# Kernel optimization log

Hardware: AMD Instinct MI355X
Metric: run time of the kernel (lower is better)

Reference implementation:

```python
import jax, jax.numpy as jnp
import numpy as np

W_RNN = 768
DEC_H = 256
TAGS = 2
TAG_EM = 32


def setup_inputs() -> dict:
    key = jax.random.key(0)
    ks = jax.random.split(key, 8)
    B, T = 64, 512
    in_size = W_RNN + TAG_EM  # 800
    aff_in = W_RNN + DEC_H    # 1024
    sents_vec = jax.random.normal(ks[0], (B, T, W_RNN), dtype=jnp.float32)
    mask_cls = jnp.ones((B, T), dtype=jnp.float32)
    # xavier-uniform-ish init for weights, zeros for biases (matches param_init)
    def xavier(k, shape):
        fan_in, fan_out = shape[1], shape[0]
        lim = float(np.sqrt(6.0 / (fan_in + fan_out)))
        return jax.random.uniform(k, shape, jnp.float32, -lim, lim)
    Wih = xavier(ks[1], (4 * DEC_H, in_size))
    Whh = xavier(ks[2], (4 * DEC_H, DEC_H))
    bih = jnp.zeros((4 * DEC_H,), jnp.float32)
    bhh = jnp.zeros((4 * DEC_H,), jnp.float32)
    Waff = xavier(ks[3], (TAGS, aff_in))
    baff = jnp.zeros((TAGS,), jnp.float32)
    tag_em = xavier(ks[4], (TAGS, TAG_EM))
    return {"sents_vec": sents_vec, "mask_cls": mask_cls, "Wih": Wih,
            "Whh": Whh, "bih": bih, "bhh": bhh, "Waff": Waff,
            "baff": baff, "tag_em": tag_em}


def reference(sents_vec, mask_cls, Wih, Whh, bih, bhh, Waff, baff, tag_em):
    # Dropout is treated in eval mode (identity), as is standard for a
    # deterministic correctness baseline.
    B, T, D = sents_vec.shape
    H = DEC_H
    h0 = jnp.zeros((B, H), sents_vec.dtype)
    go = jnp.zeros((B, TAG_EM), sents_vec.dtype)

    Hs = jnp.swapaxes(sents_vec, 0, 1)        # [T, B, D]
    Ms = jnp.swapaxes(mask_cls, 0, 1)[..., None]  # [T, B, 1]

    def step(carry, xs):
        h, c, yem = carry
        Hi, mi = xs
        x = jnp.concatenate([yem, Hi], axis=1)            # [B, 800]
        gates = x @ Wih.T + h @ Whh.T + (bih + bhh)       # [B, 4H]
        i_g, f_g, g_g, o_g = jnp.split(gates, 4, axis=1)  # torch LSTMCell order
        c_new = jax.nn.sigmoid(f_g) * c + jax.nn.sigmoid(i_g) * jnp.tanh(g_g)
        h_new = jax.nn.sigmoid(o_g) * jnp.tanh(c_new)
        score = jnp.concatenate([h_new, Hi], axis=1) @ Waff.T + baff  # [B, TAGS]
        pred = jnp.argmax(score, axis=-1)                 # [B]
        yem_new = tag_em[pred]                            # [B, TAG_EM]
        h_out = h_new * mi + h * (1.0 - mi)
        c_out = c_new * mi + c * (1.0 - mi)
        return (h_out, c_out, yem_new), score

    _, scores = jax.lax.scan(step, (h0, h0, go), (Hs, Ms))  # [T, B, TAGS]
    scores = jnp.swapaxes(scores, 0, 1)                      # [B, T, TAGS]
    return jax.nn.log_softmax(scores, axis=2)
```

## Files before the change

kernel.cpp:

```cpp
#include <hip/hip_runtime.h>
#include <cstdint>
#include <cstddef>

#define TT 512
#define BB 64
#define HH 256
#define NG 1024
#define DI 768
#define KY 32

#define LDP 56

typedef __attribute__((ext_vector_type(8))) short bfrag_t;
typedef __attribute__((ext_vector_type(4))) float f4_t;

__device__ __forceinline__ float sigf(float x) {
    return __fdividef(1.f, 1.f + __expf(-x));
}
__device__ __forceinline__ float tanhfast(float x) {
    return fmaf(2.f, sigf(2.f * x), -1.f);
}
__device__ __forceinline__ unsigned short bf_hi(float x) {
    return (unsigned short)(__float_as_uint(x) >> 16);
}
__device__ __forceinline__ float bf_hi_f(float x) {
    return __uint_as_float(__float_as_uint(x) & 0xffff0000u);
}

__global__ __launch_bounds__(256) void kgemm2(
    const float* __restrict__ sents, const float* __restrict__ Wih,
    const float* __restrict__ bih, const float* __restrict__ bhh,
    float* __restrict__ gpre, int t0)
{
    __shared__ unsigned short Ah[128 * LDP], Al[128 * LDP];
    __shared__ unsigned short Bh[128 * LDP], Bl[128 * LDP];

    const int tid = threadIdx.x;
    const int nb = blockIdx.x;
    const int mb = blockIdx.y;
    const int wv = tid >> 6, lane = tid & 63;
    const int wm = (wv >> 1) * 64, wn = (wv & 1) * 64;
    const int fl = lane & 15, quad = lane >> 4;

    f4_t acc[4][4];
#pragma unroll
    for (int mi = 0; mi < 4; ++mi)
#pragma unroll
        for (int ni = 0; ni < 4; ++ni) acc[mi][ni] = (f4_t)0.f;

    const int sr = tid >> 1, sk = (tid & 1) * 16;
    const int gr = mb * 128 + sr;
    const float* aptr = sents + ((size_t)(gr & 63) * TT + t0 + (gr >> 6)) * DI + sk;
    const float* bptr = Wih + (size_t)(nb * 128 + sr) * 800 + KY + sk;

    for (int k0 = 0; k0 < DI; k0 += 32) {
        float4 av[4], bv[4];
#pragma unroll
        for (int i = 0; i < 4; ++i) {
            av[i] = *(const float4*)(aptr + k0 + i * 4);
            bv[i] = *(const float4*)(bptr + k0 + i * 4);
        }
        __syncthreads();
#pragma unroll
        for (int i = 0; i < 4; ++i) {
            ushort4 h4, l4;
            h4.x = bf_hi(av[i].x); l4.x = bf_hi(av[i].x - bf_hi_f(av[i].x));
            h4.y = bf_hi(av[i].y); l4.y = bf_hi(av[i].y - bf_hi_f(av[i].y));
            h4.z = bf_hi(av[i].z); l4.z = bf_hi(av[i].z - bf_hi_f(av[i].z));
            h4.w = bf_hi(av[i].w); l4.w = bf_hi(av[i].w - bf_hi_f(av[i].w));
            *(ushort4*)&Ah[sr * LDP + sk + i * 4] = h4;
            *(ushort4*)&Al[sr * LDP + sk + i * 4] = l4;
            h4.x = bf_hi(bv[i].x); l4.x = bf_hi(bv[i].x - bf_hi_f(bv[i].x));
            h4.y = bf_hi(bv[i].y); l4.y = bf_hi(bv[i].y - bf_hi_f(bv[i].y));
            h4.z = bf_hi(bv[i].z); l4.z = bf_hi(bv[i].z - bf_hi_f(bv[i].z));
            h4.w = bf_hi(bv[i].w); l4.w = bf_hi(bv[i].w - bf_hi_f(bv[i].w));
            *(ushort4*)&Bh[sr * LDP + sk + i * 4] = h4;
            *(ushort4*)&Bl[sr * LDP + sk + i * 4] = l4;
        }
        __syncthreads();

        bfrag_t ah[4], al2[4], bh[4], bl2[4];
#pragma unroll
        for (int mi = 0; mi < 4; ++mi) {
            int row = wm + mi * 16 + fl;
            ah[mi]  = *(const bfrag_t*)&Ah[row * LDP + quad * 8];
            al2[mi] = *(const bfrag_t*)&Al[row * LDP + quad * 8];
        }
#pragma unroll
        for (int ni = 0; ni < 4; ++ni) {
            int col = wn + ni * 16 + fl;
            bh[ni]  = *(const bfrag_t*)&Bh[col * LDP + quad * 8];
            bl2[ni] = *(const bfrag_t*)&Bl[col * LDP + quad * 8];
        }
#pragma unroll
        for (int mi = 0; mi < 4; ++mi)
#pragma unroll
            for (int ni = 0; ni < 4; ++ni) {
                acc[mi][ni] = __builtin_amdgcn_mfma_f32_16x16x32_bf16(
                    ah[mi], bh[ni], acc[mi][ni], 0, 0, 0);
                acc[mi][ni] = __builtin_amdgcn_mfma_f32_16x16x32_bf16(
                    ah[mi], bl2[ni], acc[mi][ni], 0, 0, 0);
                acc[mi][ni] = __builtin_amdgcn_mfma_f32_16x16x32_bf16(
                    al2[mi], bh[ni], acc[mi][ni], 0, 0, 0);
            }
    }

#pragma unroll
    for (int ni = 0; ni < 4; ++ni) {
        int gcol = nb * 128 + wn + ni * 16 + fl;
        float bias = bih[gcol] + bhh[gcol];
#pragma unroll
        for (int mi = 0; mi < 4; ++mi) {
            int grow = mb * 128 + wm + mi * 16 + quad * 4;
#pragma unroll
            for (int r = 0; r < 4; ++r)
                gpre[(size_t)(grow + r) * NG + gcol] = acc[mi][ni][r] + bias;
        }
    }
}

__global__ __launch_bounds__(256) void kshi(
    const float* __restrict__ sents, const float* __restrict__ Waff,
    const float* __restrict__ baff, float* __restrict__ shi, int t0)
{
    const int tid = threadIdx.x;
    const int lane = tid & 63;
    const int r = blockIdx.x * 4 + (tid >> 6);
    const int b = r & 63, tl = r >> 6;
    const float* hi = sents + ((size_t)b * TT + t0 + tl) * DI;
    float p0 = 0.f, p1 = 0.f;
#pragma unroll
    for (int kk = 0; kk < 12; ++kk) {
        int k = kk * 64 + lane;
        float x = hi[k];
        p0 = fmaf(x, Waff[HH + k], p0);
        p1 = fmaf(x, Waff[NG + HH + k], p1);
    }
#pragma unroll
    for (int off = 32; off >= 1; off >>= 1) {
        p0 += __shfl_xor(p0, off, 64);
        p1 += __shfl_xor(p1, off, 64);
    }
    if (lane == 0) {
        shi[(size_t)r * 2 + 0] = p0 + baff[0];
        shi[(size_t)r * 2 + 1] = p1 + baff[1];
    }
}

__global__ void kinit(unsigned long long* __restrict__ hbox) {
    hbox[(size_t)blockIdx.x * 512 + threadIdx.x] = 0ull;
}

__global__ __launch_bounds__(512, 1) void krec3(
    const float* __restrict__ gpre,
    const float* __restrict__ shi,
    const float* __restrict__ Whh,
    const float* __restrict__ mask,
    float* __restrict__ out,
    float* __restrict__ sh, float* __restrict__ sc, int* __restrict__ sp,
    unsigned long long* __restrict__ hbox,
    const float* __restrict__ Wih, const float* __restrict__ tag,
    const float* __restrict__ Waff,
    int t0, int Tc, int first)
{
    const int blk = blockIdx.x;
    const int g = blk >> 6, b = blk & 63;
    const int tid = threadIdx.x;
    const int w = tid >> 6, lane = tid & 63;
    const int jl = lane & 7, kq = lane >> 3;
    const int jh = w * 8 + jl;
    const int jglob = g * 64 + jh;

    __shared__ float hk[8 * 36];
    __shared__ float hnS[HH];
    __shared__ float P[2][4][64];
    __shared__ float tg[2][KY];
    __shared__ float red[8][2];

    float4 wreg[4][8];
#pragma unroll
    for (int gt = 0; gt < 4; ++gt) {
        const float4* src = (const float4*)(Whh + (size_t)(gt * HH + jglob) * HH + kq * 32);
#pragma unroll
        for (int kk = 0; kk < 8; ++kk) wreg[gt][kk] = src[kk];
    }

    const int sdim = w * 32 + (lane & 31);
    const int stag = lane >> 5;
    const float waffR = Waff[(size_t)stag * NG + sdim];

    if (tid < 2 * KY) tg[tid >> 5][tid & 31] = tag[tid];
    __syncthreads();
    {
        int r = tid >> 8, rem = tid & 255, gt = rem >> 6, j2 = rem & 63;
        int row = gt * HH + g * 64 + j2;
        const float4* wr = (const float4*)(Wih + (size_t)row * 800);
        float s = 0.f;
#pragma unroll
        for (int kk = 0; kk < 8; ++kk) {
            float4 v = wr[kk];
            s = fmaf(v.x, tg[r][kk * 4 + 0], s);
            s = fmaf(v.y, tg[r][kk * 4 + 1], s);
            s = fmaf(v.z, tg[r][kk * 4 + 2], s);
            s = fmaf(v.w, tg[r][kk * 4 + 3], s);
        }
        P[r][gt][j2] = s;
    }

    float creg; int pred;
    if (first) {
        creg = 0.f; pred = -1;
        if (tid < 72) ((float4*)hk)[tid] = make_float4(0.f, 0.f, 0.f, 0.f);
    } else {
        creg = sc[(size_t)b * HH + jglob];
        pred = sp[b];
        if (tid < HH) hk[(tid >> 5) * 36 + (tid & 31)] = sh[(size_t)b * HH + tid];
    }
    __syncthreads();

    float cgp0, cgp1, cgp2, cgp3, cmi, cs0, cs1;
    {
        const float* gp = gpre + ((size_t)0 * BB + b) * NG;
        cgp0 = gp[0 * HH + jglob]; cgp1 = gp[1 * HH + jglob];
        cgp2 = gp[2 * HH + jglob]; cgp3 = gp[3 * HH + jglob];
        cmi = mask[(size_t)b * TT + t0];
        const float* s2 = shi + ((size_t)0 * BB + b) * 2;
        cs0 = s2[0]; cs1 = s2[1];
    }

    for (int tl = 0; tl < Tc; ++tl) {
        const int t = t0 + tl;
        const int p = t & 1;

        float pv0 = 0.f, pv1 = 0.f, pv2 = 0.f, pv3 = 0.f;
        if (pred >= 0) {
            pv0 = P[pred][0][jh]; pv1 = P[pred][1][jh];
            pv2 = P[pred][2][jh]; pv3 = P[pred][3][jh];
        }

        float a0 = 0.f, a1 = 0.f, a2 = 0.f, a3 = 0.f;
        const float4* h4 = (const float4*)(hk + kq * 36);
#pragma unroll
        for (int kk = 0; kk < 8; ++kk) {
            float4 hv = h4[kk];
            a0 = fmaf(wreg[0][kk].x, hv.x, a0); a0 = fmaf(wreg[0][kk].y, hv.y, a0);
            a0 = fmaf(wreg[0][kk].z, hv.z, a0); a0 = fmaf(wreg[0][kk].w, hv.w, a0);
            a1 = fmaf(wreg[1][kk].x, hv.x, a1); a1 = fmaf(wreg[1][kk].y, hv.y, a1);
            a1 = fmaf(wreg[1][kk].z, hv.z, a1); a1 = fmaf(wreg[1][kk].w, hv.w, a1);
            a2 = fmaf(wreg[2][kk].x, hv.x, a2); a2 = fmaf(wreg[2][kk].y, hv.y, a2);
            a2 = fmaf(wreg[2][kk].z, hv.z, a2); a2 = fmaf(wreg[2][kk].w, hv.w, a2);
            a3 = fmaf(wreg[3][kk].x, hv.x, a3); a3 = fmaf(wreg[3][kk].y, hv.y, a3);
            a3 = fmaf(wreg[3][kk].z, hv.z, a3); a3 = fmaf(wreg[3][kk].w, hv.w, a3);
        }
        a0 += __shfl_xor(a0, 8, 64); a0 += __shfl_xor(a0, 16, 64); a0 += __shfl_xor(a0, 32, 64);
        a1 += __shfl_xor(a1, 8, 64); a1 += __shfl_xor(a1, 16, 64); a1 += __shfl_xor(a1, 32, 64);
        a2 += __shfl_xor(a2, 8, 64); a2 += __shfl_xor(a2, 16, 64); a2 += __shfl_xor(a2, 32, 64);
        a3 += __shfl_xor(a3, 8, 64); a3 += __shfl_xor(a3, 16, 64); a3 += __shfl_xor(a3, 32, 64);

        float gi = a0 + cgp0 + pv0;
        float gf = a1 + cgp1 + pv1;
        float gg = a2 + cgp2 + pv2;
        float go = a3 + cgp3 + pv3;
        float ig = sigf(gi), fg = sigf(gf);
        float g2 = tanhfast(gg), og = sigf(go);
        float cn = fmaf(fg, creg, ig * g2);
        float hn = og * tanhfast(cn);
        float mi = cmi;
        float s2v0 = cs0, s2v1 = cs1;
        creg = cn * mi + creg * (1.f - mi);

        if (kq == 0) {
            unsigned long long wd =
                ((unsigned long long)__float_as_uint(hn) << 32) | (unsigned)(t + 1);
            __hip_atomic_store(&hbox[((size_t)(p * BB + b) * 4 + g) * 64 + jh], wd,
                               __ATOMIC_RELAXED, __HIP_MEMORY_SCOPE_AGENT);
            hnS[jglob] = hn;
        }

        if (tl + 1 < Tc) {
            const float* gp2 = gpre + ((size_t)(tl + 1) * BB + b) * NG;
            cgp0 = gp2[0 * HH + jglob]; cgp1 = gp2[1 * HH + jglob];
            cgp2 = gp2[2 * HH + jglob]; cgp3 = gp2[3 * HH + jglob];
            cmi = mask[(size_t)b * TT + t + 1];
            const float* s2n = shi + ((size_t)(tl + 1) * BB + b) * 2;
            cs0 = s2n[0]; cs1 = s2n[1];
        }

        if (tid < 192) {
            int pg = (g + 1 + (tid >> 6)) & 3, j2 = tid & 63;
            const unsigned long long* wp = &hbox[((size_t)(p * BB + b) * 4 + pg) * 64 + j2];
            unsigned long long wv;
            do {
                wv = __hip_atomic_load(wp, __ATOMIC_RELAXED, __HIP_MEMORY_SCOPE_AGENT);
            } while ((unsigned)wv != (unsigned)(t + 1));
            hnS[pg * 64 + j2] = __uint_as_float((unsigned)(wv >> 32));
        }
        __syncthreads();

        if (tid < HH) {
            int idx = (tid >> 5) * 36 + (tid & 31);
            float hold = hk[idx];
            hk[idx] = hnS[tid] * mi + hold * (1.f - mi);
        }
        float prod = hnS[sdim] * waffR;
        prod += __shfl_xor(prod, 1, 64);
        prod += __shfl_xor(prod, 2, 64);
        prod += __shfl_xor(prod, 4, 64);
        prod += __shfl_xor(prod, 8, 64);
        prod += __shfl_xor(prod, 16, 64);
        if ((lane & 31) == 0) red[w][stag] = prod;
        __syncthreads();

        float s0 = red[0][0];
        s0 += red[1][0]; s0 += red[2][0]; s0 += red[3][0];
        s0 += red[4][0]; s0 += red[5][0]; s0 += red[6][0]; s0 += red[7][0];
        float s1 = red[0][1];
        s1 += red[1][1]; s1 += red[2][1]; s1 += red[3][1];
        s1 += red[4][1]; s1 += red[5][1]; s1 += red[6][1]; s1 += red[7][1];
        float ts0 = s0 + s2v0, ts1 = s1 + s2v1;
        pred = (ts1 > ts0) ? 1 : 0;
        if (g == 0 && tid == 0) {
            float m = fmaxf(ts0, ts1);
            float lse = m + log1pf(expf(-fabsf(ts0 - ts1)));
            float* op = out + ((size_t)b * TT + t) * 2;
            op[0] = ts0 - lse; op[1] = ts1 - lse;
        }
    }

    if (kq == 0) {
        sh[(size_t)b * HH + jglob] = hk[(jglob >> 5) * 36 + (jglob & 31)];
        sc[(size_t)b * HH + jglob] = creg;
    }
    if (g == 0 && tid == 0) sp[b] = pred;
}

extern "C" void kernel_launch(void* const* d_in, const int* in_sizes, int n_in,
                              void* d_out, int out_size, void* d_ws, size_t ws_size,
                              hipStream_t stream) {
    (void)in_sizes; (void)n_in; (void)out_size;
    const float* sents = (const float*)d_in[0];
    const float* mask  = (const float*)d_in[1];
    const float* Wih   = (const float*)d_in[2];
    const float* Whh   = (const float*)d_in[3];
    const float* bih   = (const float*)d_in[4];
    const float* bhh   = (const float*)d_in[5];
    const float* Waff  = (const float*)d_in[6];
    const float* baff  = (const float*)d_in[7];
    const float* tag   = (const float*)d_in[8];
    float* out = (float*)d_out;

    const size_t fixed = (size_t)BB * HH * 4 * 2
                       + BB * 4
                       + (size_t)2 * BB * 4 * 64 * 8
                       + 4096;
    int Tc = 8;
    const int cands[7] = {512, 256, 128, 64, 32, 16, 8};
    for (int i = 0; i < 7; ++i) {
        size_t need = (size_t)cands[i] * BB * NG * 4
                    + (size_t)cands[i] * BB * 2 * 4
                    + fixed;
        if (need <= ws_size) { Tc = cands[i]; break; }
    }

    char* wsp = (char*)d_ws;
    float* gpre = (float*)wsp; wsp += (size_t)Tc * BB * NG * 4;
    float* shiw = (float*)wsp; wsp += (size_t)Tc * BB * 2 * 4;
    float* shst = (float*)wsp; wsp += (size_t)BB * HH * 4;
    float* scst = (float*)wsp; wsp += (size_t)BB * HH * 4;
    int*   spst = (int*)wsp;   wsp += BB * 4;
    unsigned long long* hbox = (unsigned long long*)wsp;

    kinit<<<dim3(64), 512, 0, stream>>>(hbox);

    const int nch = TT / Tc;
    for (int c = 0; c < nch; ++c) {
        const int t0 = c * Tc;
        kgemm2<<<dim3(8, Tc * 64 / 128), 256, 0, stream>>>(sents, Wih, bih, bhh, gpre, t0);
        kshi<<<dim3(Tc * 16), 256, 0, stream>>>(sents, Waff, baff, shiw, t0);
        krec3<<<dim3(256), 512, 0, stream>>>(gpre, shiw, Whh, mask, out,
                                             shst, scst, spst, hbox,
                                             Wih, tag, Waff, t0, Tc, (c == 0) ? 1 : 0);
    }
}
```

Measured before the change: 1.436 ms.

## Exchange partial affine scores via mailboxes and double-buffer h to drop a barrier

The recurrent kernel now computes each block's partial affine score over its own 64 hidden units and publishes it through a new tagged mailbox. A dedicated wave collects the four partials, so the full tag decision no longer needs a second block-wide reduction and barrier. The hidden-state buffer in shared memory is double-buffered, and masked h values are kept in registers, which removes the separate mask-mix pass and one __syncthreads per timestep. The cost is extra global atomic stores and spin-loads per step, plus a slightly different summation order for the scores.

After: 1.617 ms. 1.13x slower.

```diff
diff --git a/kernel.cpp b/kernel.cpp
--- a/kernel.cpp
+++ b/kernel.cpp
@@ -19,6 +19,9 @@
 }
 __device__ __forceinline__ float tanhfast(float x) {
     return fmaf(2.f, sigf(2.f * x), -1.f);
+}
+__device__ __forceinline__ float hmix(float hn, float hold, float mi) {
+    return fmaf(hn, mi, hold * (1.f - mi));
 }
 __device__ __forceinline__ unsigned short bf_hi(float x) {
     return (unsigned short)(__float_as_uint(x) >> 16);
@@ -147,11 +150,11 @@
     }
 }
 
-__global__ void kinit(unsigned long long* __restrict__ hbox) {
-    hbox[(size_t)blockIdx.x * 512 + threadIdx.x] = 0ull;
-}
-
-__global__ __launch_bounds__(512, 1) void krec3(
+__global__ void kinit(unsigned long long* __restrict__ box) {
+    box[(size_t)blockIdx.x * 512 + threadIdx.x] = 0ull;
+}
+
+__global__ __launch_bounds__(512, 1) void krec4(
     const float* __restrict__ gpre,
     const float* __restrict__ shi,
     const float* __restrict__ Whh,
@@ -159,6 +162,7 @@
     float* __restrict__ out,
     float* __restrict__ sh, float* __restrict__ sc, int* __restrict__ sp,
     unsigned long long* __restrict__ hbox,
+    unsigned long long* __restrict__ pbox,
     const float* __restrict__ Wih, const float* __restrict__ tag,
     const float* __restrict__ Waff,
     int t0, int Tc, int first)
@@ -170,12 +174,12 @@
     const int jl = lane & 7, kq = lane >> 3;
     const int jh = w * 8 + jl;
     const int jglob = g * 64 + jh;
-
-    __shared__ float hk[8 * 36];
-    __shared__ float hnS[HH];
+    const int pg = (g + 1 + w) & 3;
+
+    __shared__ float hk[2][8 * 36];
     __shared__ float P[2][4][64];
     __shared__ float tg[2][KY];
-    __shared__ float red[8][2];
+    __shared__ float redP[4][2];
 
     float4 wreg[4][8];
 #pragma unroll
@@ -184,10 +188,8 @@
 #pragma unroll
         for (int kk = 0; kk < 8; ++kk) wreg[gt][kk] = src[kk];
     }
-
-    const int sdim = w * 32 + (lane & 31);
-    const int stag = lane >> 5;
-    const float waffR = Waff[(size_t)stag * NG + sdim];
+    const float waff0 = Waff[jglob];
+    const float waff1 = Waff[NG + jglob];
 
     if (tid < 2 * KY) tg[tid >> 5][tid & 31] = tag[tid];
     __syncthreads();
@@ -207,30 +209,36 @@
         P[r][gt][j2] = s;
     }
 
-    float creg; int pred;
+    const int p0i = t0 & 1;
+    float creg, hreg = 0.f, hpreg = 0.f; int pred;
     if (first) {
         creg = 0.f; pred = -1;
-        if (tid < 72) ((float4*)hk)[tid] = make_float4(0.f, 0.f, 0.f, 0.f);
+        if (tid < HH) hk[p0i][(tid >> 5) * 36 + (tid & 31)] = 0.f;
     } else {
         creg = sc[(size_t)b * HH + jglob];
         pred = sp[b];
-        if (tid < HH) hk[(tid >> 5) * 36 + (tid & 31)] = sh[(size_t)b * HH + tid];
+        hreg = sh[(size_t)b * HH + jglob];
+        if (tid < 192) hpreg = sh[(size_t)b * HH + pg * 64 + lane];
+        if (tid < HH) hk[p0i][(tid >> 5) * 36 + (tid & 31)] = sh[(size_t)b * HH + tid];
     }
     __syncthreads();
 
     float cgp0, cgp1, cgp2, cgp3, cmi, cs0, cs1;
     {
-        const float* gp = gpre + ((size_t)0 * BB + b) * NG;
+        const float* gp = gpre + (size_t)b * NG;
         cgp0 = gp[0 * HH + jglob]; cgp1 = gp[1 * HH + jglob];
         cgp2 = gp[2 * HH + jglob]; cgp3 = gp[3 * HH + jglob];
         cmi = mask[(size_t)b * TT + t0];
-        const float* s2 = shi + ((size_t)0 * BB + b) * 2;
+        const float* s2 = shi + (size_t)b * 2;
         cs0 = s2[0]; cs1 = s2[1];
     }
 
     for (int tl = 0; tl < Tc; ++tl) {
         const int t = t0 + tl;
         const int p = t & 1;
+        const unsigned cnt = (unsigned)(t + 1);
+        const float* hkr = hk[p];
+        float* hkw = hk[p ^ 1];
 
         float pv0 = 0.f, pv1 = 0.f, pv2 = 0.f, pv3 = 0.f;
         if (pred >= 0) {
@@ -239,7 +247,7 @@
         }
 
         float a0 = 0.f, a1 = 0.f, a2 = 0.f, a3 = 0.f;
-        const float4* h4 = (const float4*)(hk + kq * 36);
+        const float4* h4 = (const float4*)(hkr + kq * 36);
 #pragma unroll
         for (int kk = 0; kk < 8; ++kk) {
             float4 hv = h4[kk];
@@ -265,16 +273,31 @@
         float g2 = tanhfast(gg), og = sigf(go);
         float cn = fmaf(fg, creg, ig * g2);
         float hn = og * tanhfast(cn);
-        float mi = cmi;
-        float s2v0 = cs0, s2v1 = cs1;
+        const float mi = cmi;
+        const float s2v0 = cs0, s2v1 = cs1;
         creg = cn * mi + creg * (1.f - mi);
 
         if (kq == 0) {
             unsigned long long wd =
-                ((unsigned long long)__float_as_uint(hn) << 32) | (unsigned)(t + 1);
+                ((unsigned long long)__float_as_uint(hn) << 32) | cnt;
             __hip_atomic_store(&hbox[((size_t)(p * BB + b) * 4 + g) * 64 + jh], wd,
                                __ATOMIC_RELAXED, __HIP_MEMORY_SCOPE_AGENT);
-            hnS[jglob] = hn;
+            hreg = hmix(hn, hreg, mi);
+            hkw[(jglob >> 5) * 36 + (jglob & 31)] = hreg;
+        }
+        float sp0 = hn * waff0, sp1 = hn * waff1;
+        sp0 += __shfl_xor(sp0, 1, 64); sp1 += __shfl_xor(sp1, 1, 64);
+        sp0 += __shfl_xor(sp0, 2, 64); sp1 += __shfl_xor(sp1, 2, 64);
+        sp0 += __shfl_xor(sp0, 4, 64); sp1 += __shfl_xor(sp1, 4, 64);
+        if (lane == 0) {
+            unsigned long long* pb =
+                &pbox[(((size_t)(p * BB + b) * 4 + g) * 8 + w) * 2];
+            unsigned long long w0 =
+                ((unsigned long long)__float_as_uint(sp0) << 32) | cnt;
+            unsigned long long w1 =
+                ((unsigned long long)__float_as_uint(sp1) << 32) | cnt;
+            __hip_atomic_store(&pb[0], w0, __ATOMIC_RELAXED, __HIP_MEMORY_SCOPE_AGENT);
+            __hip_atomic_store(&pb[1], w1, __ATOMIC_RELAXED, __HIP_MEMORY_SCOPE_AGENT);
         }
 
         if (tl + 1 < Tc) {
@@ -287,37 +310,36 @@
         }
 
         if (tid < 192) {
-            int pg = (g + 1 + (tid >> 6)) & 3, j2 = tid & 63;
-            const unsigned long long* wp = &hbox[((size_t)(p * BB + b) * 4 + pg) * 64 + j2];
+            const unsigned long long* wp =
+                &hbox[((size_t)(p * BB + b) * 4 + pg) * 64 + lane];
             unsigned long long wv;
             do {
                 wv = __hip_atomic_load(wp, __ATOMIC_RELAXED, __HIP_MEMORY_SCOPE_AGENT);
-            } while ((unsigned)wv != (unsigned)(t + 1));
-            hnS[pg * 64 + j2] = __uint_as_float((unsigned)(wv >> 32));
+            } while ((unsigned)wv != cnt);
+            float v = __uint_as_float((unsigned)(wv >> 32));
+            hpreg = hmix(v, hpreg, mi);
+            int kf = pg * 64 + lane;
+            hkw[(kf >> 5) * 36 + (kf & 31)] = hpreg;
+        } else if (tid < 256) {
+            int gg = lane >> 4, idx = lane & 15;
+            int sl = (g + gg) & 3;
+            const unsigned long long* wp =
+                &pbox[(((size_t)(p * BB + b) * 4 + sl) * 8 + (idx >> 1)) * 2 + (idx & 1)];
+            unsigned long long wv;
+            do {
+                wv = __hip_atomic_load(wp, __ATOMIC_RELAXED, __HIP_MEMORY_SCOPE_AGENT);
+            } while ((unsigned)wv != cnt);
+            float v = __uint_as_float((unsigned)(wv >> 32));
+            v += __shfl_xor(v, 2, 64);
+            v += __shfl_xor(v, 4, 64);
+            v += __shfl_xor(v, 8, 64);
+            if (idx < 2) redP[sl][idx] = v;
         }
         __syncthreads();
 
-        if (tid < HH) {
-            int idx = (tid >> 5) * 36 + (tid & 31);
-            float hold = hk[idx];
-            hk[idx] = hnS[tid] * mi + hold * (1.f - mi);
-        }
-        float prod = hnS[sdim] * waffR;
-        prod += __shfl_xor(prod, 1, 64);
-        prod += __shfl_xor(prod, 2, 64);
-        prod += __shfl_xor(prod, 4, 64);
-        prod += __shfl_xor(prod, 8, 64);
-        prod += __shfl_xor(prod, 16, 64);
-        if ((lane & 31) == 0) red[w][stag] = prod;
-        __syncthreads();
-
-        float s0 = red[0][0];
-        s0 += red[1][0]; s0 += red[2][0]; s0 += red[3][0];
-        s0 += red[4][0]; s0 += red[5][0]; s0 += red[6][0]; s0 += red[7][0];
-        float s1 = red[0][1];
-        s1 += red[1][1]; s1 += red[2][1]; s1 += red[3][1];
-        s1 += red[4][1]; s1 += red[5][1]; s1 += red[6][1]; s1 += red[7][1];
-        float ts0 = s0 + s2v0, ts1 = s1 + s2v1;
+        float q0 = ((redP[0][0] + redP[1][0]) + redP[2][0]) + redP[3][0];
+        float q1 = ((redP[0][1] + redP[1][1]) + redP[2][1]) + redP[3][1];
+        float ts0 = q0 + s2v0, ts1 = q1 + s2v1;
         pred = (ts1 > ts0) ? 1 : 0;
         if (g == 0 && tid == 0) {
             float m = fmaxf(ts0, ts1);
@@ -328,7 +350,7 @@
     }
 
     if (kq == 0) {
-        sh[(size_t)b * HH + jglob] = hk[(jglob >> 5) * 36 + (jglob & 31)];
+        sh[(size_t)b * HH + jglob] = hreg;
         sc[(size_t)b * HH + jglob] = creg;
     }
     if (g == 0 && tid == 0) sp[b] = pred;
@@ -352,6 +374,7 @@
     const size_t fixed = (size_t)BB * HH * 4 * 2
                        + BB * 4
                        + (size_t)2 * BB * 4 * 64 * 8
+                       + (size_t)2 * BB * 4 * 8 * 2 * 8
                        + 4096;
     int Tc = 8;
     const int cands[7] = {512, 256, 128, 64, 32, 16, 8};
@@ -368,17 +391,18 @@
     float* shst = (float*)wsp; wsp += (size_t)BB * HH * 4;
     float* scst = (float*)wsp; wsp += (size_t)BB * HH * 4;
     int*   spst = (int*)wsp;   wsp += BB * 4;
-    unsigned long long* hbox = (unsigned long long*)wsp;
-
-    kinit<<<dim3(64), 512, 0, stream>>>(hbox);
+    unsigned long long* hbox = (unsigned long long*)wsp; wsp += (size_t)2 * BB * 4 * 64 * 8;
+    unsigned long long* pbox = (unsigned long long*)wsp;
+
+    kinit<<<dim3(80), 512, 0, stream>>>(hbox);
 
     const int nch = TT / Tc;
     for (int c = 0; c < nch; ++c) {
         const int t0 = c * Tc;
         kgemm2<<<dim3(8, Tc * 64 / 128), 256, 0, stream>>>(sents, Wih, bih, bhh, gpre, t0);
         kshi<<<dim3(Tc * 16), 256, 0, stream>>>(sents, Waff, baff, shiw, t0);
-        krec3<<<dim3(256), 512, 0, stream>>>(gpre, shiw, Whh, mask, out,
-                                             shst, scst, spst, hbox,
+        krec4<<<dim3(256), 512, 0, stream>>>(gpre, shiw, Whh, mask, out,
+                                             shst, scst, spst, hbox, pbox,
                                              Wih, tag, Waff, t0, Tc, (c == 0) ? 1 : 0);
     }
 }
```

## Pre-split Wih to bf16 hi/lo once and process two batch rows per recurrence block

Applied to the files above, without the earlier changes.

Adds a kernel that converts Wih into bf16 high/low halves once per launch, so the gate GEMM loads ready-made bf16 tiles instead of splitting fp32 weights inside every tile. The recurrence kernel now handles two batch rows per block, running on 128 blocks instead of 256 and reusing the register-resident Whh slice for both rows. This halves the number of blocks that spin on the cross-block handshake and gives each block more independent work per step. In exchange, each step runs longer per block, the two batch rows are processed one after the other, and the weight split needs extra workspace.

New measurement: 1.888 ms. +31.5%, slower.

```diff
diff --git a/kernel.cpp b/kernel.cpp
--- a/kernel.cpp
+++ b/kernel.cpp
@@ -27,13 +27,25 @@
     return __uint_as_float(__float_as_uint(x) & 0xffff0000u);
 }
 
+__global__ __launch_bounds__(256) void kconvW(
+    const float* __restrict__ Wih,
+    unsigned short* __restrict__ WH, unsigned short* __restrict__ WL)
+{
+    const int col = blockIdx.x * 256 + threadIdx.x;
+    const int row = blockIdx.y;
+    float v = Wih[(size_t)row * 800 + KY + col];
+    WH[(size_t)row * DI + col] = bf_hi(v);
+    WL[(size_t)row * DI + col] = bf_hi(v - bf_hi_f(v));
+}
+
 __global__ __launch_bounds__(256) void kgemm2(
-    const float* __restrict__ sents, const float* __restrict__ Wih,
+    const float* __restrict__ sents,
+    const unsigned short* __restrict__ WH, const unsigned short* __restrict__ WL,
     const float* __restrict__ bih, const float* __restrict__ bhh,
     float* __restrict__ gpre, int t0)
 {
-    __shared__ unsigned short Ah[128 * LDP], Al[128 * LDP];
-    __shared__ unsigned short Bh[128 * LDP], Bl[128 * LDP];
+    __shared__ __align__(16) unsigned short Ah[128 * LDP], Al[128 * LDP];
+    __shared__ __align__(16) unsigned short Bh[128 * LDP], Bl[128 * LDP];
 
     const int tid = threadIdx.x;
     const int nb = blockIdx.x;
@@ -51,15 +63,17 @@
     const int sr = tid >> 1, sk = (tid & 1) * 16;
     const int gr = mb * 128 + sr;
     const float* aptr = sents + ((size_t)(gr & 63) * TT + t0 + (gr >> 6)) * DI + sk;
-    const float* bptr = Wih + (size_t)(nb * 128 + sr) * 800 + KY + sk;
+    const unsigned short* bhp = WH + (size_t)(nb * 128 + sr) * DI + sk;
+    const unsigned short* blp = WL + (size_t)(nb * 128 + sr) * DI + sk;
 
     for (int k0 = 0; k0 < DI; k0 += 32) {
-        float4 av[4], bv[4];
-#pragma unroll
-        for (int i = 0; i < 4; ++i) {
-            av[i] = *(const float4*)(aptr + k0 + i * 4);
-            bv[i] = *(const float4*)(bptr + k0 + i * 4);
-        }
+        float4 av[4];
+#pragma unroll
+        for (int i = 0; i < 4; ++i) av[i] = *(const float4*)(aptr + k0 + i * 4);
+        uint4 bh0 = *(const uint4*)(bhp + k0);
+        uint4 bh1 = *(const uint4*)(bhp + k0 + 8);
+        uint4 bl0 = *(const uint4*)(blp + k0);
+        uint4 bl1 = *(const uint4*)(blp + k0 + 8);
         __syncthreads();
 #pragma unroll
         for (int i = 0; i < 4; ++i) {
@@ -70,13 +84,11 @@
             h4.w = bf_hi(av[i].w); l4.w = bf_hi(av[i].w - bf_hi_f(av[i].w));
             *(ushort4*)&Ah[sr * LDP + sk + i * 4] = h4;
             *(ushort4*)&Al[sr * LDP + sk + i * 4] = l4;
-            h4.x = bf_hi(bv[i].x); l4.x = bf_hi(bv[i].x - bf_hi_f(bv[i].x));
-            h4.y = bf_hi(bv[i].y); l4.y = bf_hi(bv[i].y - bf_hi_f(bv[i].y));
-            h4.z = bf_hi(bv[i].z); l4.z = bf_hi(bv[i].z - bf_hi_f(bv[i].z));
-            h4.w = bf_hi(bv[i].w); l4.w = bf_hi(bv[i].w - bf_hi_f(bv[i].w));
-            *(ushort4*)&Bh[sr * LDP + sk + i * 4] = h4;
-            *(ushort4*)&Bl[sr * LDP + sk + i * 4] = l4;
-        }
+        }
+        *(uint4*)&Bh[sr * LDP + sk + 0] = bh0;
+        *(uint4*)&Bh[sr * LDP + sk + 8] = bh1;
+        *(uint4*)&Bl[sr * LDP + sk + 0] = bl0;
+        *(uint4*)&Bl[sr * LDP + sk + 8] = bl1;
         __syncthreads();
 
         bfrag_t ah[4], al2[4], bh[4], bl2[4];
@@ -151,7 +163,7 @@
     hbox[(size_t)blockIdx.x * 512 + threadIdx.x] = 0ull;
 }
 
-__global__ __launch_bounds__(512, 1) void krec3(
+__global__ __launch_bounds__(512, 1) void krec5(
     const float* __restrict__ gpre,
     const float* __restrict__ shi,
     const float* __restrict__ Whh,
@@ -164,18 +176,19 @@
     int t0, int Tc, int first)
 {
     const int blk = blockIdx.x;
-    const int g = blk >> 6, b = blk & 63;
+    const int g = blk >> 5, bp = blk & 31;
+    const int b0 = bp, b1 = bp + 32;
     const int tid = threadIdx.x;
     const int w = tid >> 6, lane = tid & 63;
     const int jl = lane & 7, kq = lane >> 3;
     const int jh = w * 8 + jl;
     const int jglob = g * 64 + jh;
 
-    __shared__ float hk[8 * 36];
-    __shared__ float hnS[HH];
+    __shared__ float hk0[8 * 36], hk1[8 * 36];
+    __shared__ float hnS0[HH], hnS1[HH];
     __shared__ float P[2][4][64];
     __shared__ float tg[2][KY];
-    __shared__ float red[8][2];
+    __shared__ float red0[8][2], red1[8][2];
 
     float4 wreg[4][8];
 #pragma unroll
@@ -207,131 +220,247 @@
         P[r][gt][j2] = s;
     }
 
-    float creg; int pred;
+    float creg0, creg1; int pred0, pred1;
     if (first) {
-        creg = 0.f; pred = -1;
-        if (tid < 72) ((float4*)hk)[tid] = make_float4(0.f, 0.f, 0.f, 0.f);
+        creg0 = 0.f; creg1 = 0.f; pred0 = -1; pred1 = -1;
+        if (tid < HH) {
+            hk0[(tid >> 5) * 36 + (tid & 31)] = 0.f;
+            hk1[(tid >> 5) * 36 + (tid & 31)] = 0.f;
+        }
     } else {
-        creg = sc[(size_t)b * HH + jglob];
-        pred = sp[b];
-        if (tid < HH) hk[(tid >> 5) * 36 + (tid & 31)] = sh[(size_t)b * HH + tid];
+        creg0 = sc[(size_t)b0 * HH + jglob];
+        creg1 = sc[(size_t)b1 * HH + jglob];
+        pred0 = sp[b0]; pred1 = sp[b1];
+        if (tid < HH) {
+            hk0[(tid >> 5) * 36 + (tid & 31)] = sh[(size_t)b0 * HH + tid];
+            hk1[(tid >> 5) * 36 + (tid & 31)] = sh[(size_t)b1 * HH + tid];
+        }
     }
     __syncthreads();
 
-    float cgp0, cgp1, cgp2, cgp3, cmi, cs0, cs1;
+    float cgp00, cgp01, cgp02, cgp03, cmi0, cs00, cs01;
+    float cgp10, cgp11, cgp12, cgp13, cmi1, cs10, cs11;
     {
-        const float* gp = gpre + ((size_t)0 * BB + b) * NG;
-        cgp0 = gp[0 * HH + jglob]; cgp1 = gp[1 * HH + jglob];
-        cgp2 = gp[2 * HH + jglob]; cgp3 = gp[3 * HH + jglob];
-        cmi = mask[(size_t)b * TT + t0];
-        const float* s2 = shi + ((size_t)0 * BB + b) * 2;
-        cs0 = s2[0]; cs1 = s2[1];
+        const float* gpa = gpre + (size_t)b0 * NG;
+        cgp00 = gpa[0 * HH + jglob]; cgp01 = gpa[1 * HH + jglob];
+        cgp02 = gpa[2 * HH + jglob]; cgp03 = gpa[3 * HH + jglob];
+        cmi0 = mask[(size_t)b0 * TT + t0];
+        const float* s2a = shi + (size_t)b0 * 2;
+        cs00 = s2a[0]; cs01 = s2a[1];
+        const float* gpb = gpre + (size_t)b1 * NG;
+        cgp10 = gpb[0 * HH + jglob]; cgp11 = gpb[1 * HH + jglob];
+        cgp12 = gpb[2 * HH + jglob]; cgp13 = gpb[3 * HH + jglob];
+        cmi1 = mask[(size_t)b1 * TT + t0];
+        const float* s2b = shi + (size_t)b1 * 2;
+        cs10 = s2b[0]; cs11 = s2b[1];
     }
 
     for (int tl = 0; tl < Tc; ++tl) {
         const int t = t0 + tl;
         const int p = t & 1;
+        const unsigned cnt = (unsigned)(t + 1);
 
         float pv0 = 0.f, pv1 = 0.f, pv2 = 0.f, pv3 = 0.f;
-        if (pred >= 0) {
-            pv0 = P[pred][0][jh]; pv1 = P[pred][1][jh];
-            pv2 = P[pred][2][jh]; pv3 = P[pred][3][jh];
-        }
-
+        if (pred0 >= 0) {
+            pv0 = P[pred0][0][jh]; pv1 = P[pred0][1][jh];
+            pv2 = P[pred0][2][jh]; pv3 = P[pred0][3][jh];
+        }
         float a0 = 0.f, a1 = 0.f, a2 = 0.f, a3 = 0.f;
-        const float4* h4 = (const float4*)(hk + kq * 36);
-#pragma unroll
-        for (int kk = 0; kk < 8; ++kk) {
-            float4 hv = h4[kk];
-            a0 = fmaf(wreg[0][kk].x, hv.x, a0); a0 = fmaf(wreg[0][kk].y, hv.y, a0);
-            a0 = fmaf(wreg[0][kk].z, hv.z, a0); a0 = fmaf(wreg[0][kk].w, hv.w, a0);
-            a1 = fmaf(wreg[1][kk].x, hv.x, a1); a1 = fmaf(wreg[1][kk].y, hv.y, a1);
-            a1 = fmaf(wreg[1][kk].z, hv.z, a1); a1 = fmaf(wreg[1][kk].w, hv.w, a1);
-            a2 = fmaf(wreg[2][kk].x, hv.x, a2); a2 = fmaf(wreg[2][kk].y, hv.y, a2);
-            a2 = fmaf(wreg[2][kk].z, hv.z, a2); a2 = fmaf(wreg[2][kk].w, hv.w, a2);
-            a3 = fmaf(wreg[3][kk].x, hv.x, a3); a3 = fmaf(wreg[3][kk].y, hv.y, a3);
-            a3 = fmaf(wreg[3][kk].z, hv.z, a3); a3 = fmaf(wreg[3][kk].w, hv.w, a3);
+        {
+            const float4* h4 = (const float4*)(hk0 + kq * 36);
+#pragma unroll
+            for (int kk = 0; kk < 8; ++kk) {
+                float4 hv = h4[kk];
+                a0 = fmaf(wreg[0][kk].x, hv.x, a0); a0 = fmaf(wreg[0][kk].y, hv.y, a0);
+                a0 = fmaf(wreg[0][kk].z, hv.z, a0); a0 = fmaf(wreg[0][kk].w, hv.w, a0);
+                a1 = fmaf(wreg[1][kk].x, hv.x, a1); a1 = fmaf(wreg[1][kk].y, hv.y, a1);
+                a1 = fmaf(wreg[1][kk].z, hv.z, a1); a1 = fmaf(wreg[1][kk].w, hv.w, a1);
+                a2 = fmaf(wreg[2][kk].x, hv.x, a2); a2 = fmaf(wreg[2][kk].y, hv.y, a2);
+                a2 = fmaf(wreg[2][kk].z, hv.z, a2); a2 = fmaf(wreg[2][kk].w, hv.w, a2);
+                a3 = fmaf(wreg[3][kk].x, hv.x, a3); a3 = fmaf(wreg[3][kk].y, hv.y, a3);
+                a3 = fmaf(wreg[3][kk].z, hv.z, a3); a3 = fmaf(wreg[3][kk].w, hv.w, a3);
+            }
         }
         a0 += __shfl_xor(a0, 8, 64); a0 += __shfl_xor(a0, 16, 64); a0 += __shfl_xor(a0, 32, 64);
         a1 += __shfl_xor(a1, 8, 64); a1 += __shfl_xor(a1, 16, 64); a1 += __shfl_xor(a1, 32, 64);
         a2 += __shfl_xor(a2, 8, 64); a2 += __shfl_xor(a2, 16, 64); a2 += __shfl_xor(a2, 32, 64);
         a3 += __shfl_xor(a3, 8, 64); a3 += __shfl_xor(a3, 16, 64); a3 += __shfl_xor(a3, 32, 64);
 
-        float gi = a0 + cgp0 + pv0;
-        float gf = a1 + cgp1 + pv1;
-        float gg = a2 + cgp2 + pv2;
-        float go = a3 + cgp3 + pv3;
-        float ig = sigf(gi), fg = sigf(gf);
-        float g2 = tanhfast(gg), og = sigf(go);
-        float cn = fmaf(fg, creg, ig * g2);
-        float hn = og * tanhfast(cn);
-        float mi = cmi;
-        float s2v0 = cs0, s2v1 = cs1;
-        creg = cn * mi + creg * (1.f - mi);
-
+        const float mi0 = cmi0, sv00 = cs00, sv01 = cs01;
+        float hn0;
+        {
+            float gi = a0 + cgp00 + pv0;
+            float gf = a1 + cgp01 + pv1;
+            float gg = a2 + cgp02 + pv2;
+            float go = a3 + cgp03 + pv3;
+            float ig = sigf(gi), fg = sigf(gf);
+            float g2 = tanhfast(gg), og = sigf(go);
+            float cn = fmaf(fg, creg0, ig * g2);
+            hn0 = og * tanhfast(cn);
+            creg0 = cn * mi0 + creg0 * (1.f - mi0);
+        }
         if (kq == 0) {
             unsigned long long wd =
-                ((unsigned long long)__float_as_uint(hn) << 32) | (unsigned)(t + 1);
-            __hip_atomic_store(&hbox[((size_t)(p * BB + b) * 4 + g) * 64 + jh], wd,
+                ((unsigned long long)__float_as_uint(hn0) << 32) | cnt;
+            __hip_atomic_store(&hbox[((size_t)(p * BB + b0) * 4 + g) * 64 + jh], wd,
                                __ATOMIC_RELAXED, __HIP_MEMORY_SCOPE_AGENT);
-            hnS[jglob] = hn;
+            hnS0[jglob] = hn0;
+        }
+
+        float qv0 = 0.f, qv1 = 0.f, qv2 = 0.f, qv3 = 0.f;
+        if (pred1 >= 0) {
+            qv0 = P[pred1][0][jh]; qv1 = P[pred1][1][jh];
+            qv2 = P[pred1][2][jh]; qv3 = P[pred1][3][jh];
+        }
+        float e0 = 0.f, e1 = 0.f, e2 = 0.f, e3 = 0.f;
+        {
+            const float4* h4 = (const float4*)(hk1 + kq * 36);
+#pragma unroll
+            for (int kk = 0; kk < 8; ++kk) {
+                float4 hv = h4[kk];
+                e0 = fmaf(wreg[0][kk].x, hv.x, e0); e0 = fmaf(wreg[0][kk].y, hv.y, e0);
+                e0 = fmaf(wreg[0][kk].z, hv.z, e0); e0 = fmaf(wreg[0][kk].w, hv.w, e0);
+                e1 = fmaf(wreg[1][kk].x, hv.x, e1); e1 = fmaf(wreg[1][kk].y, hv.y, e1);
+                e1 = fmaf(wreg[1][kk].z, hv.z, e1); e1 = fmaf(wreg[1][kk].w, hv.w, e1);
+                e2 = fmaf(wreg[2][kk].x, hv.x, e2); e2 = fmaf(wreg[2][kk].y, hv.y, e2);
+                e2 = fmaf(wreg[2][kk].z, hv.z, e2); e2 = fmaf(wreg[2][kk].w, hv.w, e2);
+                e3 = fmaf(wreg[3][kk].x, hv.x, e3); e3 = fmaf(wreg[3][kk].y, hv.y, e3);
+                e3 = fmaf(wreg[3][kk].z, hv.z, e3); e3 = fmaf(wreg[3][kk].w, hv.w, e3);
+            }
+        }
+        e0 += __shfl_xor(e0, 8, 64); e0 += __shfl_xor(e0, 16, 64); e0 += __shfl_xor(e0, 32, 64);
+        e1 += __shfl_xor(e1, 8, 64); e1 += __shfl_xor(e1, 16, 64); e1 += __shfl_xor(e1, 32, 64);
+        e2 += __shfl_xor(e2, 8, 64); e2 += __shfl_xor(e2, 16, 64); e2 += __shfl_xor(e2, 32, 64);
+        e3 += __shfl_xor(e3, 8, 64); e3 += __shfl_xor(e3, 16, 64); e3 += __shfl_xor(e3, 32, 64);
+
+        const float mi1 = cmi1, sv10 = cs10, sv11 = cs11;
+        float hn1;
+        {
+            float gi = e0 + cgp10 + qv0;
+            float gf = e1 + cgp11 + qv1;
+            float gg = e2 + cgp12 + qv2;
+            float go = e3 + cgp13 + qv3;
+            float ig = sigf(gi), fg = sigf(gf);
+            float g2 = tanhfast(gg), og = sigf(go);
+            float cn = fmaf(fg, creg1, ig * g2);
+            hn1 = og * tanhfast(cn);
+            creg1 = cn * mi1 + creg1 * (1.f - mi1);
+        }
+        if (kq == 0) {
+            unsigned long long wd =
+                ((unsigned long long)__float_as_uint(hn1) << 32) | cnt;
+            __hip_atomic_store(&hbox[((size_t)(p * BB + b1) * 4 + g) * 64 + jh], wd,
+                               __ATOMIC_RELAXED, __HIP_MEMORY_SCOPE_AGENT);
+            hnS1[jglob] = hn1;
         }
 
         if (tl + 1 < Tc) {
-            const float* gp2 = gpre + ((size_t)(tl + 1) * BB + b) * NG;
-            cgp0 = gp2[0 * HH + jglob]; cgp1 = gp2[1 * HH + jglob];
-            cgp2 = gp2[2 * HH + jglob]; cgp3 = gp2[3 * HH + jglob];
-            cmi = mask[(size_t)b * TT + t + 1];
-            const float* s2n = shi + ((size_t)(tl + 1) * BB + b) * 2;
-            cs0 = s2n[0]; cs1 = s2n[1];
+            const float* gpa = gpre + ((size_t)(tl + 1) * BB + b0) * NG;
+            cgp00 = gpa[0 * HH + jglob]; cgp01 = gpa[1 * HH + jglob];
+            cgp02 = gpa[2 * HH + jglob]; cgp03 = gpa[3 * HH + jglob];
+            cmi0 = mask[(size_t)b0 * TT + t + 1];
+            const float* s2a = shi + ((size_t)(tl + 1) * BB + b0) * 2;
+            cs00 = s2a[0]; cs01 = s2a[1];
+            const float* gpb = gpre + ((size_t)(tl + 1) * BB + b1) * NG;
+            cgp10 = gpb[0 * HH + jglob]; cgp11 = gpb[1 * HH + jglob];
+            cgp12 = gpb[2 * HH + jglob]; cgp13 = gpb[3 * HH + jglob];
+            cmi1 = mask[(size_t)b1 * TT + t + 1];
+            const float* s2b = shi + ((size_t)(tl + 1) * BB + b1) * 2;
+            cs10 = s2b[0]; cs11 = s2b[1];
         }
 
         if (tid < 192) {
             int pg = (g + 1 + (tid >> 6)) & 3, j2 = tid & 63;
-            const unsigned long long* wp = &hbox[((size_t)(p * BB + b) * 4 + pg) * 64 + j2];
-            unsigned long long wv;
-            do {
-                wv = __hip_atomic_load(wp, __ATOMIC_RELAXED, __HIP_MEMORY_SCOPE_AGENT);
-            } while ((unsigned)wv != (unsigned)(t + 1));
-            hnS[pg * 64 + j2] = __uint_as_float((unsigned)(wv >> 32));
+            {
+                const unsigned long long* wp =
+                    &hbox[((size_t)(p * BB + b0) * 4 + pg) * 64 + j2];
+                unsigned long long wv;
+                do {
+                    wv = __hip_atomic_load(wp, __ATOMIC_RELAXED, __HIP_MEMORY_SCOPE_AGENT);
+                } while ((unsigned)wv != cnt);
+                hnS0[pg * 64 + j2] = __uint_as_float((unsigned)(wv >> 32));
+            }
+            {
+                const unsigned long long* wp =
+                    &hbox[((size_t)(p * BB + b1) * 4 + pg) * 64 + j2];
+                unsigned long long wv;
+                do {
+                    wv = __hip_atomic_load(wp, __ATOMIC_RELAXED, __HIP_MEMORY_SCOPE_AGENT);
+                } while ((unsigned)wv != cnt);
+                hnS1[pg * 64 + j2] = __uint_as_float((unsigned)(wv >> 32));
+            }
         }
         __syncthreads();
 
         if (tid < HH) {
             int idx = (tid >> 5) * 36 + (tid & 31);
-            float hold = hk[idx];
-            hk[idx] = hnS[tid] * mi + hold * (1.f - mi);
-        }
-        float prod = hnS[sdim] * waffR;
-        prod += __shfl_xor(prod, 1, 64);
-        prod += __shfl_xor(prod, 2, 64);
-        prod += __shfl_xor(prod, 4, 64);
-        prod += __shfl_xor(prod, 8, 64);
-        prod += __shfl_xor(prod, 16, 64);
-        if ((lane & 31) == 0) red[w][stag] = prod;
+            float hold = hk0[idx];
+            hk0[idx] = hnS0[tid] * mi0 + hold * (1.f - mi0);
+        } else {
+            int d = tid - HH;
+            int idx = (d >> 5) * 36 + (d & 31);
+            float hold = hk1[idx];
+            hk1[idx] = hnS1[d] * mi1 + hold * (1.f - mi1);
+        }
+        float pr0 = hnS0[sdim] * waffR;
+        pr0 += __shfl_xor(pr0, 1, 64);
+        pr0 += __shfl_xor(pr0, 2, 64);
+        pr0 += __shfl_xor(pr0, 4, 64);
+        pr0 += __shfl_xor(pr0, 8, 64);
+        pr0 += __shfl_xor(pr0, 16, 64);
+        float pr1 = hnS1[sdim] * waffR;
+        pr1 += __shfl_xor(pr1, 1, 64);
+        pr1 += __shfl_xor(pr1, 2, 64);
+        pr1 += __shfl_xor(pr1, 4, 64);
+        pr1 += __shfl_xor(pr1, 8, 64);
+        pr1 += __shfl_xor(pr1, 16, 64);
+        if ((lane & 31) == 0) {
+            red0[w][stag] = pr0;
+            red1[w][stag] = pr1;
+        }
         __syncthreads();
 
-        float s0 = red[0][0];
-        s0 += red[1][0]; s0 += red[2][0]; s0 += red[3][0];
-        s0 += red[4][0]; s0 += red[5][0]; s0 += red[6][0]; s0 += red[7][0];
-        float s1 = red[0][1];
-        s1 += red[1][1]; s1 += red[2][1]; s1 += red[3][1];
-        s1 += red[4][1]; s1 += red[5][1]; s1 += red[6][1]; s1 += red[7][1];
-        float ts0 = s0 + s2v0, ts1 = s1 + s2v1;
-        pred = (ts1 > ts0) ? 1 : 0;
-        if (g == 0 && tid == 0) {
-            float m = fmaxf(ts0, ts1);
-            float lse = m + log1pf(expf(-fabsf(ts0 - ts1)));
-            float* op = out + ((size_t)b * TT + t) * 2;
-            op[0] = ts0 - lse; op[1] = ts1 - lse;
+        {
+            float s0 = red0[0][0];
+            s0 += red0[1][0]; s0 += red0[2][0]; s0 += red0[3][0];
+            s0 += red0[4][0]; s0 += red0[5][0]; s0 += red0[6][0]; s0 += red0[7][0];
+            float s1 = red0[0][1];
+            s1 += red0[1][1]; s1 += red0[2][1]; s1 += red0[3][1];
+            s1 += red0[4][1]; s1 += red0[5][1]; s1 += red0[6][1]; s1 += red0[7][1];
+            float ts0 = s0 + sv00, ts1 = s1 + sv01;
+            pred0 = (ts1 > ts0) ? 1 : 0;
+            if (g == 0 && tid == 0) {
+                float m = fmaxf(ts0, ts1);
+                float lse = m + log1pf(expf(-fabsf(ts0 - ts1)));
+                float* op = out + ((size_t)b0 * TT + t) * 2;
+                op[0] = ts0 - lse; op[1] = ts1 - lse;
+            }
+        }
+        {
+            float s0 = red1[0][0];
+            s0 += red1[1][0]; s0 += red1[2][0]; s0 += red1[3][0];
+            s0 += red1[4][0]; s0 += red1[5][0]; s0 += red1[6][0]; s0 += red1[7][0];
+            float s1 = red1[0][1];
+            s1 += red1[1][1]; s1 += red1[2][1]; s1 += red1[3][1];
+            s1 += red1[4][1]; s1 += red1[5][1]; s1 += red1[6][1]; s1 += red1[7][1];
+            float ts0 = s0 + sv10, ts1 = s1 + sv11;
+            pred1 = (ts1 > ts0) ? 1 : 0;
+            if (g == 0 && tid == 0) {
+                float m = fmaxf(ts0, ts1);
+                float lse = m + log1pf(expf(-fabsf(ts0 - ts1)));
+                float* op = out + ((size_t)b1 * TT + t) * 2;
+                op[0] = ts0 - lse; op[1] = ts1 - lse;
+            }
         }
     }
 
     if (kq == 0) {
-        sh[(size_t)b * HH + jglob] = hk[(jglob >> 5) * 36 + (jglob & 31)];
-        sc[(size_t)b * HH + jglob] = creg;
-    }
-    if (g == 0 && tid == 0) sp[b] = pred;
+        sh[(size_t)b0 * HH + jglob] = hk0[(jglob >> 5) * 36 + (jglob & 31)];
+        sc[(size_t)b0 * HH + jglob] = creg0;
+        sh[(size_t)b1 * HH + jglob] = hk1[(jglob >> 5) * 36 + (jglob & 31)];
+        sc[(size_t)b1 * HH + jglob] = creg1;
+    }
+    if (g == 0 && tid == 0) { sp[b0] = pred0; sp[b1] = pred1; }
 }
 
 extern "C" void kernel_launch(void* const* d_in, const int* in_sizes, int n_in,
@@ -349,7 +478,9 @@
     const float* tag   = (const float*)d_in[8];
     float* out = (float*)d_out;
 
-    const size_t fixed = (size_t)BB * HH * 4 * 2
+    const size_t wsplit = (size_t)NG * DI * 2 * 2;
+    const size_t fixed = wsplit
+                       + (size_t)BB * HH * 4 * 2
                        + BB * 4
                        + (size_t)2 * BB * 4 * 64 * 8
                        + 4096;
@@ -363,6 +494,8 @@
     }
 
     char* wsp = (char*)d_ws;
+    unsigned short* WH = (unsigned short*)wsp; wsp += (size_t)NG * DI * 2;
+    unsigned short* WL = (unsigned short*)wsp; wsp += (size_t)NG * DI * 2;
     float* gpre = (float*)wsp; wsp += (size_t)Tc * BB * NG * 4;
     float* shiw = (float*)wsp; wsp += (size_t)Tc * BB * 2 * 4;
     float* shst = (float*)wsp; wsp += (size_t)BB * HH * 4;
@@ -370,14 +503,15 @@
     int*   spst = (int*)wsp;   wsp += BB * 4;
     unsigned long long* hbox = (unsigned long long*)wsp;
 
+    kconvW<<<dim3(3, 1024), 256, 0, stream>>>(Wih, WH, WL);
     kinit<<<dim3(64), 512, 0, stream>>>(hbox);
 
     const int nch = TT / Tc;
     for (int c = 0; c < nch; ++c) {
         const int t0 = c * Tc;
-        kgemm2<<<dim3(8, Tc * 64 / 128), 256, 0, stream>>>(sents, Wih, bih, bhh, gpre, t0);
+        kgemm2<<<dim3(8, Tc * 64 / 128), 256, 0, stream>>>(sents, WH, WL, bih, bhh, gpre, t0);
         kshi<<<dim3(Tc * 16), 256, 0, stream>>>(sents, Waff, baff, shiw, t0);
-        krec3<<<dim3(256), 512, 0, stream>>>(gpre, shiw, Whh, mask, out,
+        krec5<<<dim3(128), 512, 0, stream>>>(gpre, shiw, Whh, mask, out,
                                              shst, scst, spst, hbox,
                                              Wih, tag, Waff, t0, Tc, (c == 0) ? 1 : 0);
     }
```
